# Performance work log

Hardware: AMD Instinct MI355X
Metric: run time of the kernel (lower is better)

Reference implementation:

```python
import jax, jax.numpy as jnp
import numpy as np

N_NODES = 100000
N_EDGES = 1250000
D = 64
N_LAYERS = 4


def setup_inputs() -> dict:
    key = jax.random.key(0)
    ks = jax.random.split(key, 6)
    x = jax.random.normal(ks[0], (N_NODES, D), dtype=jnp.float32)
    edge_index = jax.random.randint(ks[1], (2, N_EDGES), 0, N_NODES, dtype=jnp.int64)
    s = 1.0 / np.sqrt(D)
    # PyG SAGEConv per layer: lin_l (applied to aggregated neighbors, with bias)
    # and lin_r (applied to self features, no bias). All layers are 64->64, so stack.
    Wl = jax.random.uniform(ks[2], (N_LAYERS, D, D), dtype=jnp.float32, minval=-s, maxval=s)
    bl = jax.random.uniform(ks[3], (N_LAYERS, D), dtype=jnp.float32, minval=-s, maxval=s)
    Wr = jax.random.uniform(ks[4], (N_LAYERS, D, D), dtype=jnp.float32, minval=-s, maxval=s)
    return {"x": x, "edge_index": edge_index, "Wl": Wl, "bl": bl, "Wr": Wr}


def reference(x, edge_index, Wl, bl, Wr):
    src = edge_index[0]  # message source: x_j
    dst = edge_index[1]  # aggregate at target node
    h = x
    for i in range(N_LAYERS):
        msg = h[src]  # [E, D] irregular gather
        agg = jax.ops.segment_max(msg, dst, num_segments=N_NODES)  # max-pool aggregation
        agg = jnp.where(jnp.isneginf(agg), 0.0, agg)  # empty segments -> 0 (PyG convention)
        h = jax.nn.relu(agg @ Wl[i] + bl[i] + h @ Wr[i])
    return h
```

## Files before the change

kernel.cpp:

```cpp
#include <hip/hip_runtime.h>
#include <hip/hip_fp16.h>
#include <stdint.h>

#define NN 100000
#define NE 1250000
#define DD 64
#define NL 4

#define NPART3 64
#define PSIZE3 1563
#define TILE4 1024
#define NTB ((NE / 4 + TILE4 - 1) / TILE4)
#define SCANA_N (NPART3 * NTB)
#define SRCBITS 17

#define MB2 64
#define L2BLOCKS ((NN + MB2 - 1) / MB2)
#define APAD 136
#define CPADH 72
#define CPADF 68

typedef _Float16 half8 __attribute__((ext_vector_type(8)));
typedef _Float16 half2v __attribute__((ext_vector_type(2)));
typedef float floatx4 __attribute__((ext_vector_type(4)));
typedef int intx4 __attribute__((ext_vector_type(4)));

__device__ __forceinline__ unsigned f2h2(float a, float b) {
    __half2 h = __floats2half2_rn(a, b);
    return *reinterpret_cast<unsigned*>(&h);
}
__device__ __forceinline__ unsigned umax2(unsigned a, unsigned b) {
    half2v x = *reinterpret_cast<half2v*>(&a);
    half2v y = *reinterpret_cast<half2v*>(&b);
    half2v r = __builtin_elementwise_max(x, y);
    return *reinterpret_cast<unsigned*>(&r);
}

__global__ __launch_bounds__(256) void cast_kernel(const float* __restrict__ x,
                                                   __half* __restrict__ hh) {
    int i = blockIdx.x * 256 + threadIdx.x;
    float4 v = ((const float4*)x)[i];
    uint2 u;
    u.x = f2h2(v.x, v.y);
    u.y = f2h2(v.z, v.w);
    ((uint2*)hh)[i] = u;
}

__global__ __launch_bounds__(256) void countA_kernel(const int* __restrict__ dst,
                                                     int* __restrict__ blockcnt) {
    __shared__ int cnt[NPART3];
    int tid = threadIdx.x;
    if (tid < NPART3) cnt[tid] = 0;
    __syncthreads();
    int b = blockIdx.x;
    #pragma unroll
    for (int r = 0; r < 4; ++r) {
        int i4 = b * TILE4 + r * 256 + tid;
        if (i4 < NE / 4) {
            intx4 d = __builtin_nontemporal_load(&((const intx4*)dst)[i4]);
            atomicAdd(&cnt[(unsigned)d.x / PSIZE3], 1);
            atomicAdd(&cnt[(unsigned)d.y / PSIZE3], 1);
            atomicAdd(&cnt[(unsigned)d.z / PSIZE3], 1);
            atomicAdd(&cnt[(unsigned)d.w / PSIZE3], 1);
        }
    }
    __syncthreads();
    if (tid < NPART3) blockcnt[tid * NTB + b] = cnt[tid];
}

__global__ __launch_bounds__(1024) void scanA_kernel(int* __restrict__ blockcnt) {
    __shared__ int sm[1024];
    int tid = threadIdx.x;
    int base = tid * 20;
    int e[20];
    int s = 0;
    #pragma unroll
    for (int j = 0; j < 20; ++j) {
        e[j] = (base + j < SCANA_N) ? blockcnt[base + j] : 0;
        s += e[j];
    }
    sm[tid] = s;
    __syncthreads();
    for (int off = 1; off < 1024; off <<= 1) {
        int v = (tid >= off) ? sm[tid - off] : 0;
        __syncthreads();
        sm[tid] += v;
        __syncthreads();
    }
    int run = sm[tid] - s;
    #pragma unroll
    for (int j = 0; j < 20; ++j) {
        if (base + j < SCANA_N) {
            blockcnt[base + j] = run;
            run += e[j];
        }
    }
}

__global__ __launch_bounds__(256) void scatterA_kernel(const int* __restrict__ src,
                                                       const int* __restrict__ dst,
                                                       const int* __restrict__ blockcnt,
                                                       int* __restrict__ ebufP) {
    __shared__ int cur[NPART3];
    int tid = threadIdx.x;
    int b = blockIdx.x;
    if (tid < NPART3) cur[tid] = blockcnt[tid * NTB + b];
    __syncthreads();
    #pragma unroll
    for (int r = 0; r < 4; ++r) {
        int i4 = b * TILE4 + r * 256 + tid;
        if (i4 < NE / 4) {
            intx4 d = __builtin_nontemporal_load(&((const intx4*)dst)[i4]);
            intx4 s = __builtin_nontemporal_load(&((const intx4*)src)[i4]);
            int part, p;
            part = (unsigned)d.x / PSIZE3; p = atomicAdd(&cur[part], 1);
            ebufP[p] = ((d.x - part * PSIZE3) << SRCBITS) | s.x;
            part = (unsigned)d.y / PSIZE3; p = atomicAdd(&cur[part], 1);
            ebufP[p] = ((d.y - part * PSIZE3) << SRCBITS) | s.y;
            part = (unsigned)d.z / PSIZE3; p = atomicAdd(&cur[part], 1);
            ebufP[p] = ((d.z - part * PSIZE3) << SRCBITS) | s.z;
            part = (unsigned)d.w / PSIZE3; p = atomicAdd(&cur[part], 1);
            ebufP[p] = ((d.w - part * PSIZE3) << SRCBITS) | s.w;
        }
    }
}

__global__ __launch_bounds__(1024) void fillD_kernel(const int* __restrict__ ebufP,
                                                     const int* __restrict__ blockcnt,
                                                     int* __restrict__ row_start,
                                                     int* __restrict__ csr) {
    __shared__ int cnt[PSIZE3];
    __shared__ int localstart[PSIZE3];
    __shared__ int partial[1024];
    int part = blockIdx.x;
    int tid = threadIdx.x;
    int nbase = part * PSIZE3;
    int base = blockcnt[part * NTB];
    int hi = (part < NPART3 - 1) ? blockcnt[(part + 1) * NTB] : NE;

    for (int j = tid; j < PSIZE3; j += 1024) cnt[j] = 0;
    __syncthreads();

    for (int i = base + tid; i < hi; i += 1024)
        atomicAdd(&cnt[(unsigned)ebufP[i] >> SRCBITS], 1);
    __syncthreads();

    int j0 = tid * 2;
    int e0 = (j0 < PSIZE3) ? cnt[j0] : 0;
    int e1 = (j0 + 1 < PSIZE3) ? cnt[j0 + 1] : 0;
    int s = e0 + e1;
    partial[tid] = s;
    __syncthreads();
    for (int off = 1; off < 1024; off <<= 1) {
        int v = (tid >= off) ? partial[tid - off] : 0;
        __syncthreads();
        partial[tid] += v;
        __syncthreads();
    }
    int run = partial[tid] - s;
    if (j0 < PSIZE3) localstart[j0] = run;
    if (j0 + 1 < PSIZE3) localstart[j0 + 1] = run + e0;
    __syncthreads();

    int nmax = NN - nbase; if (nmax > PSIZE3) nmax = PSIZE3;
    for (int j = tid; j < nmax; j += 1024)
        row_start[nbase + j] = base + localstart[j];
    if (part == NPART3 - 1 && tid == 0) row_start[NN] = NE;

    for (int j = tid; j < PSIZE3; j += 1024) cnt[j] = 0;
    __syncthreads();

    for (int i = base + tid; i < hi; i += 1024) {
        int p = ebufP[i];
        int dl = (unsigned)p >> SRCBITS;
        int local = atomicAdd(&cnt[dl], 1);
        csr[base + localstart[dl] + local] = p & ((1 << SRCBITS) - 1);
    }
}

__global__ __launch_bounds__(256) void agg_kernel(const __half* __restrict__ hh,
                                                  const int* __restrict__ row_start,
                                                  const int* __restrict__ csr,
                                                  __half* __restrict__ aggh) {
    int tid = threadIdx.x;
    int wv = tid >> 6;
    int lane = tid & 63;
    int g = lane >> 3;
    int c8 = (lane & 7) * 8;
    int n0 = blockIdx.x * 8 + wv * 2;
    int n1 = n0 + 1;
    int base0 = row_start[n0];
    int base1 = row_start[n1];
    int cnt0 = base1 - base0;
    int cnt1 = row_start[n1 + 1] - base1;
    int cl0 = cnt0 - 1;
    int cl1 = cnt1 - 1;

    int idx0 = 0, idx1 = 0;
    if (cnt0 > 0) idx0 = csr[base0 + ((lane <= cl0) ? lane : cl0)];
    if (cnt1 > 0) idx1 = csr[base1 + ((lane <= cl1) ? lane : cl1)];

    const uint4 NI4 = make_uint4(0xFC00FC00u, 0xFC00FC00u, 0xFC00FC00u, 0xFC00FC00u);
    uint4 acc0 = (cnt0 > 0) ? NI4 : make_uint4(0, 0, 0, 0);
    uint4 acc1 = (cnt1 > 0) ? NI4 : make_uint4(0, 0, 0, 0);

    int m0 = (cnt0 < 64) ? cnt0 : 64;
    int m1 = (cnt1 < 64) ? cnt1 : 64;
    int kmax = (m0 > m1) ? m0 : m1;

    for (int k = 0; k < kmax; k += 16) {
        int ka = k + g;
        int kb = k + g + 8;
        int s00 = 0, s01 = 0, s10 = 0, s11 = 0;
        if (cnt0 > 0) {
            s00 = __shfl(idx0, (ka <= cl0) ? ka : cl0, 64);
            s01 = __shfl(idx0, (kb <= cl0) ? kb : cl0, 64);
        }
        if (cnt1 > 0) {
            s10 = __shfl(idx1, (ka <= cl1) ? ka : cl1, 64);
            s11 = __shfl(idx1, (kb <= cl1) ? kb : cl1, 64);
        }
        if (ka < m0) {
            uint4 u = *(const uint4*)&hh[(size_t)s00 * DD + c8];
            acc0.x = umax2(acc0.x, u.x); acc0.y = umax2(acc0.y, u.y);
            acc0.z = umax2(acc0.z, u.z); acc0.w = umax2(acc0.w, u.w);
        }
        if (ka < m1) {
            uint4 u = *(const uint4*)&hh[(size_t)s10 * DD + c8];
            acc1.x = umax2(acc1.x, u.x); acc1.y = umax2(acc1.y, u.y);
            acc1.z = umax2(acc1.z, u.z); acc1.w = umax2(acc1.w, u.w);
        }
        if (kb < m0) {
            uint4 u = *(const uint4*)&hh[(size_t)s01 * DD + c8];
            acc0.x = umax2(acc0.x, u.x); acc0.y = umax2(acc0.y, u.y);
            acc0.z = umax2(acc0.z, u.z); acc0.w = umax2(acc0.w, u.w);
        }
        if (kb < m1) {
            uint4 u = *(const uint4*)&hh[(size_t)s11 * DD + c8];
            acc1.x = umax2(acc1.x, u.x); acc1.y = umax2(acc1.y, u.y);
            acc1.z = umax2(acc1.z, u.z); acc1.w = umax2(acc1.w, u.w);
        }
    }
    for (int k = 64 + g; k < cnt0; k += 8) {
        int s = csr[base0 + k];
        uint4 u = *(const uint4*)&hh[(size_t)s * DD + c8];
        acc0.x = umax2(acc0.x, u.x); acc0.y = umax2(acc0.y, u.y);
        acc0.z = umax2(acc0.z, u.z); acc0.w = umax2(acc0.w, u.w);
    }
    for (int k = 64 + g; k < cnt1; k += 8) {
        int s = csr[base1 + k];
        uint4 u = *(const uint4*)&hh[(size_t)s * DD + c8];
        acc1.x = umax2(acc1.x, u.x); acc1.y = umax2(acc1.y, u.y);
        acc1.z = umax2(acc1.z, u.z); acc1.w = umax2(acc1.w, u.w);
    }

    #pragma unroll
    for (int off = 8; off <= 32; off <<= 1) {
        acc0.x = umax2(acc0.x, (unsigned)__shfl_xor((int)acc0.x, off, 64));
        acc0.y = umax2(acc0.y, (unsigned)__shfl_xor((int)acc0.y, off, 64));
        acc0.z = umax2(acc0.z, (unsigned)__shfl_xor((int)acc0.z, off, 64));
        acc0.w = umax2(acc0.w, (unsigned)__shfl_xor((int)acc0.w, off, 64));
        acc1.x = umax2(acc1.x, (unsigned)__shfl_xor((int)acc1.x, off, 64));
        acc1.y = umax2(acc1.y, (unsigned)__shfl_xor((int)acc1.y, off, 64));
        acc1.z = umax2(acc1.z, (unsigned)__shfl_xor((int)acc1.z, off, 64));
        acc1.w = umax2(acc1.w, (unsigned)__shfl_xor((int)acc1.w, off, 64));
    }
    if (lane < 8) {
        *(uint4*)&aggh[(size_t)n0 * DD + c8] = acc0;
        *(uint4*)&aggh[(size_t)n1 * DD + c8] = acc1;
    }
}

__global__ __launch_bounds__(256, 4) void layer_mfma_kernel(
        const __half* __restrict__ aggh,
        __half* __restrict__ hh,
        float* __restrict__ hout,
        const float* __restrict__ Wl,
        const float* __restrict__ bl,
        const float* __restrict__ Wr,
        int last) {
    __shared__ char smem[2 * MB2 * APAD * 2];
    _Float16* a_s  = (_Float16*)smem;
    _Float16* bt_s = (_Float16*)(smem + MB2 * APAD * 2);

    int tid = threadIdx.x;
    int lane = tid & 63;
    int w = tid >> 6;
    int node0 = blockIdx.x * MB2;

    #pragma unroll
    for (int i = 0; i < 4; ++i) {
        int idx = i * 256 + tid;
        int r = idx >> 4;
        int c4 = idx & 15;
        int node = node0 + r; if (node > NN - 1) node = NN - 1;
        const __half* srcp = (c4 < 8) ? (aggh + (size_t)node * DD + c4 * 8)
                                      : (hh + (size_t)node * DD + (c4 - 8) * 8);
        uint4 v = *(const uint4*)srcp;
        *(uint4*)&a_s[r * APAD + c4 * 8] = v;
    }
    {
        int n = tid & 63;
        int kb = tid >> 6;
        #pragma unroll
        for (int kk = 0; kk < 32; ++kk) {
            int k = kb * 32 + kk;
            float wv = (k < 64) ? Wl[k * DD + n] : Wr[(k - 64) * DD + n];
            bt_s[n * APAD + k] = (_Float16)wv;
        }
    }
    __syncthreads();

    floatx4 acc[4];
    #pragma unroll
    for (int nt = 0; nt < 4; ++nt) acc[nt] = (floatx4){0.f, 0.f, 0.f, 0.f};
    int m = lane & 15;
    int q = lane >> 4;

    #pragma unroll
    for (int ks = 0; ks < 4; ++ks) {
        half8 af = *(half8*)&a_s[(w * 16 + m) * APAD + q * 8 + ks * 32];
        #pragma unroll
        for (int nt = 0; nt < 4; ++nt) {
            half8 bf = *(half8*)&bt_s[(nt * 16 + m) * APAD + q * 8 + ks * 32];
            acc[nt] = __builtin_amdgcn_mfma_f32_16x16x32_f16(af, bf, acc[nt], 0, 0, 0);
        }
    }
    __syncthreads();

    _Float16* ch = (_Float16*)smem;
    float*    cf = (float*)(smem + MB2 * CPADH * 2);

    #pragma unroll
    for (int nt = 0; nt < 4; ++nt) {
        int col = nt * 16 + m;
        float b = bl[col];
        #pragma unroll
        for (int r = 0; r < 4; ++r) {
            int rowl = w * 16 + q * 4 + r;
            float o = fmaxf(acc[nt][r] + b, 0.0f);
            ch[rowl * CPADH + col] = (_Float16)o;
            if (last) cf[rowl * CPADF + col] = o;
        }
    }
    __syncthreads();

    #pragma unroll
    for (int i = 0; i < 2; ++i) {
        int idx = i * 256 + tid;
        int r = idx >> 3;
        int c4 = idx & 7;
        int node = node0 + r;
        if (node < NN) {
            uint4 v = *(uint4*)&ch[r * CPADH + c4 * 8];
            *(uint4*)&hh[(size_t)node * DD + c4 * 8] = v;
        }
    }
    if (last) {
        #pragma unroll
        for (int i = 0; i < 4; ++i) {
            int idx = i * 256 + tid;
            int r = idx >> 4;
            int c4 = idx & 15;
            int node = node0 + r;
            if (node < NN) {
                float4 v = *(float4*)&cf[r * CPADF + c4 * 4];
                *(float4*)&hout[(size_t)node * DD + c4 * 4] = v;
            }
        }
    }
}

extern "C" void kernel_launch(void* const* d_in, const int* in_sizes, int n_in,
                              void* d_out, int out_size, void* d_ws, size_t ws_size,
                              hipStream_t stream) {
    const float* x  = (const float*)d_in[0];
    const int*   ei = (const int*)d_in[1];
    const float* Wl = (const float*)d_in[2];
    const float* bl = (const float*)d_in[3];
    const float* Wr = (const float*)d_in[4];
    float* h = (float*)d_out;

    const int* src = ei;
    const int* dst = ei + NE;

    char* ws = (char*)d_ws;
    __half* aggh     = (__half*)ws;  ws += (size_t)NN * DD * sizeof(__half);
    __half* hh       = (__half*)ws;  ws += (size_t)NN * DD * sizeof(__half);
    int* row_start   = (int*)ws;     ws += (size_t)(NN + 16) * sizeof(int);
    int* blockcnt    = (int*)ws;     ws += (size_t)(SCANA_N + 16) * sizeof(int);
    int* csr         = (int*)ws;

    int* ebufP = (int*)aggh;

    cast_kernel<<<(NN * DD / 4) / 256, 256, 0, stream>>>(x, hh);

    countA_kernel<<<NTB, 256, 0, stream>>>(dst, blockcnt);
    scanA_kernel<<<1, 1024, 0, stream>>>(blockcnt);
    scatterA_kernel<<<NTB, 256, 0, stream>>>(src, dst, blockcnt, ebufP);
    fillD_kernel<<<NPART3, 1024, 0, stream>>>(ebufP, blockcnt, row_start, csr);

    for (int l = 0; l < NL; ++l) {
        agg_kernel<<<NN / 8, 256, 0, stream>>>(hh, row_start, csr, aggh);
        layer_mfma_kernel<<<L2BLOCKS, 256, 0, stream>>>(
            aggh, hh, h, Wl + (size_t)l * DD * DD, bl + (size_t)l * DD, Wr + (size_t)l * DD * DD,
            (l == NL - 1) ? 1 : 0);
    }
}
```

Before: 301.2 us.

## Fuse neighbor max-aggregation into per-layer MFMA kernel with ping-pong buffers

Merges the separate aggregation kernel into the layer GEMM kernel. Each wave gathers and max-reduces neighbors for its 16 nodes straight into shared memory before the MFMA, and hidden states ping-pong between two half buffers. This removes the aggh round trip through global memory and one launch per layer. The last layer now writes only the fp32 output, not the unused fp16 copy. In exchange, each fused block holds more registers (16 index slots per lane) with fewer waves per node, which may reduce latency hiding for the irregular gathers.

```diff
diff --git a/kernel.cpp b/kernel.cpp
--- a/kernel.cpp
+++ b/kernel.cpp
@@ -178,102 +178,11 @@
     }
 }
 
-__global__ __launch_bounds__(256) void agg_kernel(const __half* __restrict__ hh,
-                                                  const int* __restrict__ row_start,
-                                                  const int* __restrict__ csr,
-                                                  __half* __restrict__ aggh) {
-    int tid = threadIdx.x;
-    int wv = tid >> 6;
-    int lane = tid & 63;
-    int g = lane >> 3;
-    int c8 = (lane & 7) * 8;
-    int n0 = blockIdx.x * 8 + wv * 2;
-    int n1 = n0 + 1;
-    int base0 = row_start[n0];
-    int base1 = row_start[n1];
-    int cnt0 = base1 - base0;
-    int cnt1 = row_start[n1 + 1] - base1;
-    int cl0 = cnt0 - 1;
-    int cl1 = cnt1 - 1;
-
-    int idx0 = 0, idx1 = 0;
-    if (cnt0 > 0) idx0 = csr[base0 + ((lane <= cl0) ? lane : cl0)];
-    if (cnt1 > 0) idx1 = csr[base1 + ((lane <= cl1) ? lane : cl1)];
-
-    const uint4 NI4 = make_uint4(0xFC00FC00u, 0xFC00FC00u, 0xFC00FC00u, 0xFC00FC00u);
-    uint4 acc0 = (cnt0 > 0) ? NI4 : make_uint4(0, 0, 0, 0);
-    uint4 acc1 = (cnt1 > 0) ? NI4 : make_uint4(0, 0, 0, 0);
-
-    int m0 = (cnt0 < 64) ? cnt0 : 64;
-    int m1 = (cnt1 < 64) ? cnt1 : 64;
-    int kmax = (m0 > m1) ? m0 : m1;
-
-    for (int k = 0; k < kmax; k += 16) {
-        int ka = k + g;
-        int kb = k + g + 8;
-        int s00 = 0, s01 = 0, s10 = 0, s11 = 0;
-        if (cnt0 > 0) {
-            s00 = __shfl(idx0, (ka <= cl0) ? ka : cl0, 64);
-            s01 = __shfl(idx0, (kb <= cl0) ? kb : cl0, 64);
-        }
-        if (cnt1 > 0) {
-            s10 = __shfl(idx1, (ka <= cl1) ? ka : cl1, 64);
-            s11 = __shfl(idx1, (kb <= cl1) ? kb : cl1, 64);
-        }
-        if (ka < m0) {
-            uint4 u = *(const uint4*)&hh[(size_t)s00 * DD + c8];
-            acc0.x = umax2(acc0.x, u.x); acc0.y = umax2(acc0.y, u.y);
-            acc0.z = umax2(acc0.z, u.z); acc0.w = umax2(acc0.w, u.w);
-        }
-        if (ka < m1) {
-            uint4 u = *(const uint4*)&hh[(size_t)s10 * DD + c8];
-            acc1.x = umax2(acc1.x, u.x); acc1.y = umax2(acc1.y, u.y);
-            acc1.z = umax2(acc1.z, u.z); acc1.w = umax2(acc1.w, u.w);
-        }
-        if (kb < m0) {
-            uint4 u = *(const uint4*)&hh[(size_t)s01 * DD + c8];
-            acc0.x = umax2(acc0.x, u.x); acc0.y = umax2(acc0.y, u.y);
-            acc0.z = umax2(acc0.z, u.z); acc0.w = umax2(acc0.w, u.w);
-        }
-        if (kb < m1) {
-            uint4 u = *(const uint4*)&hh[(size_t)s11 * DD + c8];
-            acc1.x = umax2(acc1.x, u.x); acc1.y = umax2(acc1.y, u.y);
-            acc1.z = umax2(acc1.z, u.z); acc1.w = umax2(acc1.w, u.w);
-        }
-    }
-    for (int k = 64 + g; k < cnt0; k += 8) {
-        int s = csr[base0 + k];
-        uint4 u = *(const uint4*)&hh[(size_t)s * DD + c8];
-        acc0.x = umax2(acc0.x, u.x); acc0.y = umax2(acc0.y, u.y);
-        acc0.z = umax2(acc0.z, u.z); acc0.w = umax2(acc0.w, u.w);
-    }
-    for (int k = 64 + g; k < cnt1; k += 8) {
-        int s = csr[base1 + k];
-        uint4 u = *(const uint4*)&hh[(size_t)s * DD + c8];
-        acc1.x = umax2(acc1.x, u.x); acc1.y = umax2(acc1.y, u.y);
-        acc1.z = umax2(acc1.z, u.z); acc1.w = umax2(acc1.w, u.w);
-    }
-
-    #pragma unroll
-    for (int off = 8; off <= 32; off <<= 1) {
-        acc0.x = umax2(acc0.x, (unsigned)__shfl_xor((int)acc0.x, off, 64));
-        acc0.y = umax2(acc0.y, (unsigned)__shfl_xor((int)acc0.y, off, 64));
-        acc0.z = umax2(acc0.z, (unsigned)__shfl_xor((int)acc0.z, off, 64));
-        acc0.w = umax2(acc0.w, (unsigned)__shfl_xor((int)acc0.w, off, 64));
-        acc1.x = umax2(acc1.x, (unsigned)__shfl_xor((int)acc1.x, off, 64));
-        acc1.y = umax2(acc1.y, (unsigned)__shfl_xor((int)acc1.y, off, 64));
-        acc1.z = umax2(acc1.z, (unsigned)__shfl_xor((int)acc1.z, off, 64));
-        acc1.w = umax2(acc1.w, (unsigned)__shfl_xor((int)acc1.w, off, 64));
-    }
-    if (lane < 8) {
-        *(uint4*)&aggh[(size_t)n0 * DD + c8] = acc0;
-        *(uint4*)&aggh[(size_t)n1 * DD + c8] = acc1;
-    }
-}
-
-__global__ __launch_bounds__(256, 4) void layer_mfma_kernel(
-        const __half* __restrict__ aggh,
-        __half* __restrict__ hh,
+__global__ __launch_bounds__(256, 4) void layer_fused_kernel(
+        const __half* __restrict__ hin,
+        const int* __restrict__ row_start,
+        const int* __restrict__ csr,
+        __half* __restrict__ hnext,
         float* __restrict__ hout,
         const float* __restrict__ Wl,
         const float* __restrict__ bl,
@@ -288,16 +197,14 @@
     int w = tid >> 6;
     int node0 = blockIdx.x * MB2;
 
-    #pragma unroll
-    for (int i = 0; i < 4; ++i) {
+    uint4 selfv[2];
+    #pragma unroll
+    for (int i = 0; i < 2; ++i) {
         int idx = i * 256 + tid;
-        int r = idx >> 4;
-        int c4 = idx & 15;
+        int r = idx >> 3;
+        int c4 = idx & 7;
         int node = node0 + r; if (node > NN - 1) node = NN - 1;
-        const __half* srcp = (c4 < 8) ? (aggh + (size_t)node * DD + c4 * 8)
-                                      : (hh + (size_t)node * DD + (c4 - 8) * 8);
-        uint4 v = *(const uint4*)srcp;
-        *(uint4*)&a_s[r * APAD + c4 * 8] = v;
+        selfv[i] = *(const uint4*)(hin + (size_t)node * DD + c4 * 8);
     }
     {
         int n = tid & 63;
@@ -309,54 +216,163 @@
             bt_s[n * APAD + k] = (_Float16)wv;
         }
     }
-    __syncthreads();
-
-    floatx4 acc[4];
-    #pragma unroll
-    for (int nt = 0; nt < 4; ++nt) acc[nt] = (floatx4){0.f, 0.f, 0.f, 0.f};
-    int m = lane & 15;
-    int q = lane >> 4;
-
-    #pragma unroll
-    for (int ks = 0; ks < 4; ++ks) {
-        half8 af = *(half8*)&a_s[(w * 16 + m) * APAD + q * 8 + ks * 32];
-        #pragma unroll
-        for (int nt = 0; nt < 4; ++nt) {
-            half8 bf = *(half8*)&bt_s[(nt * 16 + m) * APAD + q * 8 + ks * 32];
-            acc[nt] = __builtin_amdgcn_mfma_f32_16x16x32_f16(af, bf, acc[nt], 0, 0, 0);
-        }
-    }
-    __syncthreads();
-
-    _Float16* ch = (_Float16*)smem;
-    float*    cf = (float*)(smem + MB2 * CPADH * 2);
-
-    #pragma unroll
-    for (int nt = 0; nt < 4; ++nt) {
-        int col = nt * 16 + m;
-        float b = bl[col];
-        #pragma unroll
-        for (int r = 0; r < 4; ++r) {
-            int rowl = w * 16 + q * 4 + r;
-            float o = fmaxf(acc[nt][r] + b, 0.0f);
-            ch[rowl * CPADH + col] = (_Float16)o;
-            if (last) cf[rowl * CPADF + col] = o;
-        }
-    }
-    __syncthreads();
+
+    int wbase = node0 + w * 16;
+    int ii = wbase + ((lane < 17) ? lane : 16);
+    if (ii > NN) ii = NN;
+    int rsl = row_start[ii];
+
+    int idxA[16];
+    #pragma unroll
+    for (int j = 0; j < 16; ++j) {
+        int bj = __shfl(rsl, j, 64);
+        int cj = __shfl(rsl, j + 1, 64) - bj;
+        idxA[j] = (cj > 0) ? csr[bj + ((lane < cj) ? lane : (cj - 1))] : 0;
+    }
+
+    int g = lane >> 3;
+    int c8 = (lane & 7) * 8;
+    const uint4 NI4 = make_uint4(0xFC00FC00u, 0xFC00FC00u, 0xFC00FC00u, 0xFC00FC00u);
+
+    #pragma unroll
+    for (int t = 0; t < 8; ++t) {
+        const int j0 = 2 * t;
+        const int j1 = 2 * t + 1;
+        int base0 = __shfl(rsl, j0, 64);
+        int cnt0  = __shfl(rsl, j0 + 1, 64) - base0;
+        int base1 = __shfl(rsl, j1, 64);
+        int cnt1  = __shfl(rsl, j1 + 1, 64) - base1;
+        int cl0 = cnt0 - 1;
+        int cl1 = cnt1 - 1;
+        int idx0 = idxA[j0];
+        int idx1 = idxA[j1];
+
+        uint4 acc0 = (cnt0 > 0) ? NI4 : make_uint4(0, 0, 0, 0);
+        uint4 acc1 = (cnt1 > 0) ? NI4 : make_uint4(0, 0, 0, 0);
+
+        int m0 = (cnt0 < 64) ? cnt0 : 64;
+        int m1 = (cnt1 < 64) ? cnt1 : 64;
+        int kmax = (m0 > m1) ? m0 : m1;
+
+        for (int k = 0; k < kmax; k += 16) {
+            int ka = k + g;
+            int kb = k + g + 8;
+            int s00 = 0, s01 = 0, s10 = 0, s11 = 0;
+            if (cnt0 > 0) {
+                s00 = __shfl(idx0, (ka <= cl0) ? ka : cl0, 64);
+                s01 = __shfl(idx0, (kb <= cl0) ? kb : cl0, 64);
+            }
+            if (cnt1 > 0) {
+                s10 = __shfl(idx1, (ka <= cl1) ? ka : cl1, 64);
+                s11 = __shfl(idx1, (kb <= cl1) ? kb : cl1, 64);
+            }
+            if (ka < m0) {
+                uint4 u = *(const uint4*)&hin[(size_t)s00 * DD + c8];
+                acc0.x = umax2(acc0.x, u.x); acc0.y = umax2(acc0.y, u.y);
+                acc0.z = umax2(acc0.z, u.z); acc0.w = umax2(acc0.w, u.w);
+            }
+            if (ka < m1) {
+                uint4 u = *(const uint4*)&hin[(size_t)s10 * DD + c8];
+                acc1.x = umax2(acc1.x, u.x); acc1.y = umax2(acc1.y, u.y);
+                acc1.z = umax2(acc1.z, u.z); acc1.w = umax2(acc1.w, u.w);
+            }
+            if (kb < m0) {
+                uint4 u = *(const uint4*)&hin[(size_t)s01 * DD + c8];
+                acc0.x = umax2(acc0.x, u.x); acc0.y = umax2(acc0.y, u.y);
+                acc0.z = umax2(acc0.z, u.z); acc0.w = umax2(acc0.w, u.w);
+            }
+            if (kb < m1) {
+                uint4 u = *(const uint4*)&hin[(size_t)s11 * DD + c8];
+                acc1.x = umax2(acc1.x, u.x); acc1.y = umax2(acc1.y, u.y);
+                acc1.z = umax2(acc1.z, u.z); acc1.w = umax2(acc1.w, u.w);
+            }
+        }
+        for (int k = 64 + g; k < cnt0; k += 8) {
+            int s = csr[base0 + k];
+            uint4 u = *(const uint4*)&hin[(size_t)s * DD + c8];
+            acc0.x = umax2(acc0.x, u.x); acc0.y = umax2(acc0.y, u.y);
+            acc0.z = umax2(acc0.z, u.z); acc0.w = umax2(acc0.w, u.w);
+        }
+        for (int k = 64 + g; k < cnt1; k += 8) {
+            int s = csr[base1 + k];
+            uint4 u = *(const uint4*)&hin[(size_t)s * DD + c8];
+            acc1.x = umax2(acc1.x, u.x); acc1.y = umax2(acc1.y, u.y);
+            acc1.z = umax2(acc1.z, u.z); acc1.w = umax2(acc1.w, u.w);
+        }
+
+        #pragma unroll
+        for (int off = 8; off <= 32; off <<= 1) {
+            acc0.x = umax2(acc0.x, (unsigned)__shfl_xor((int)acc0.x, off, 64));
+            acc0.y = umax2(acc0.y, (unsigned)__shfl_xor((int)acc0.y, off, 64));
+            acc0.z = umax2(acc0.z, (unsigned)__shfl_xor((int)acc0.z, off, 64));
+            acc0.w = umax2(acc0.w, (unsigned)__shfl_xor((int)acc0.w, off, 64));
+            acc1.x = umax2(acc1.x, (unsigned)__shfl_xor((int)acc1.x, off, 64));
+            acc1.y = umax2(acc1.y, (unsigned)__shfl_xor((int)acc1.y, off, 64));
+            acc1.z = umax2(acc1.z, (unsigned)__shfl_xor((int)acc1.z, off, 64));
+            acc1.w = umax2(acc1.w, (unsigned)__shfl_xor((int)acc1.w, off, 64));
+        }
+        if (lane < 8) {
+            *(uint4*)&a_s[(w * 16 + j0) * APAD + c8] = acc0;
+            *(uint4*)&a_s[(w * 16 + j1) * APAD + c8] = acc1;
+        }
+    }
 
     #pragma unroll
     for (int i = 0; i < 2; ++i) {
         int idx = i * 256 + tid;
         int r = idx >> 3;
         int c4 = idx & 7;
-        int node = node0 + r;
-        if (node < NN) {
-            uint4 v = *(uint4*)&ch[r * CPADH + c4 * 8];
-            *(uint4*)&hh[(size_t)node * DD + c4 * 8] = v;
-        }
-    }
-    if (last) {
+        *(uint4*)&a_s[r * APAD + 64 + c4 * 8] = selfv[i];
+    }
+    __syncthreads();
+
+    floatx4 acc[4];
+    #pragma unroll
+    for (int nt = 0; nt < 4; ++nt) acc[nt] = (floatx4){0.f, 0.f, 0.f, 0.f};
+    int m = lane & 15;
+    int q = lane >> 4;
+
+    #pragma unroll
+    for (int ks = 0; ks < 4; ++ks) {
+        half8 af = *(half8*)&a_s[(w * 16 + m) * APAD + q * 8 + ks * 32];
+        #pragma unroll
+        for (int nt = 0; nt < 4; ++nt) {
+            half8 bf = *(half8*)&bt_s[(nt * 16 + m) * APAD + q * 8 + ks * 32];
+            acc[nt] = __builtin_amdgcn_mfma_f32_16x16x32_f16(af, bf, acc[nt], 0, 0, 0);
+        }
+    }
+    __syncthreads();
+
+    _Float16* ch = (_Float16*)smem;
+    float*    cf = (float*)(smem + MB2 * CPADH * 2);
+
+    #pragma unroll
+    for (int nt = 0; nt < 4; ++nt) {
+        int col = nt * 16 + m;
+        float b = bl[col];
+        #pragma unroll
+        for (int r = 0; r < 4; ++r) {
+            int rowl = w * 16 + q * 4 + r;
+            float o = fmaxf(acc[nt][r] + b, 0.0f);
+            if (last) cf[rowl * CPADF + col] = o;
+            else      ch[rowl * CPADH + col] = (_Float16)o;
+        }
+    }
+    __syncthreads();
+
+    if (!last) {
+        #pragma unroll
+        for (int i = 0; i < 2; ++i) {
+            int idx = i * 256 + tid;
+            int r = idx >> 3;
+            int c4 = idx & 7;
+            int node = node0 + r;
+            if (node < NN) {
+                uint4 v = *(uint4*)&ch[r * CPADH + c4 * 8];
+                *(uint4*)&hnext[(size_t)node * DD + c4 * 8] = v;
+            }
+        }
+    } else {
         #pragma unroll
         for (int i = 0; i < 4; ++i) {
             int idx = i * 256 + tid;
@@ -385,25 +401,26 @@
     const int* dst = ei + NE;
 
     char* ws = (char*)d_ws;
-    __half* aggh     = (__half*)ws;  ws += (size_t)NN * DD * sizeof(__half);
-    __half* hh       = (__half*)ws;  ws += (size_t)NN * DD * sizeof(__half);
+    __half* hb1      = (__half*)ws;  ws += (size_t)NN * DD * sizeof(__half);
+    __half* hb0      = (__half*)ws;  ws += (size_t)NN * DD * sizeof(__half);
     int* row_start   = (int*)ws;     ws += (size_t)(NN + 16) * sizeof(int);
     int* blockcnt    = (int*)ws;     ws += (size_t)(SCANA_N + 16) * sizeof(int);
     int* csr         = (int*)ws;
 
-    int* ebufP = (int*)aggh;
-
-    cast_kernel<<<(NN * DD / 4) / 256, 256, 0, stream>>>(x, hh);
+    int* ebufP = (int*)hb1;
+
+    cast_kernel<<<(NN * DD / 4) / 256, 256, 0, stream>>>(x, hb0);
 
     countA_kernel<<<NTB, 256, 0, stream>>>(dst, blockcnt);
     scanA_kernel<<<1, 1024, 0, stream>>>(blockcnt);
     scatterA_kernel<<<NTB, 256, 0, stream>>>(src, dst, blockcnt, ebufP);
     fillD_kernel<<<NPART3, 1024, 0, stream>>>(ebufP, blockcnt, row_start, csr);
 
+    __half* bufs[2] = { hb0, hb1 };
     for (int l = 0; l < NL; ++l) {
-        agg_kernel<<<NN / 8, 256, 0, stream>>>(hh, row_start, csr, aggh);
-        layer_mfma_kernel<<<L2BLOCKS, 256, 0, stream>>>(
-            aggh, hh, h, Wl + (size_t)l * DD * DD, bl + (size_t)l * DD, Wr + (size_t)l * DD * DD,
+        layer_fused_kernel<<<L2BLOCKS, 256, 0, stream>>>(
+            bufs[l & 1], row_start, csr, bufs[(l + 1) & 1], h,
+            Wl + (size_t)l * DD * DD, bl + (size_t)l * DD, Wr + (size_t)l * DD * DD,
             (l == NL - 1) ? 1 : 0);
     }
 }
```

New measurement: 353.9 us. +17.5%, slower.
